# Kernel tuning notes

Hardware: AMD Instinct MI355X
Metric: run time of the kernel (lower is better)

## Reference

```python
import jax, jax.numpy as jnp
import numpy as np


def setup_inputs() -> dict:
    key = jax.random.key(0)
    k1, k2, k3, k4, k5 = jax.random.split(key, 5)
    B, T, N, F_IN, F_OUT, N_TYPES = 32, 128, 32, 256, 256, 8
    inp = jax.random.normal(k1, (B, T, N, F_IN), dtype=jnp.float32)
    g = jax.random.uniform(k2, (N, N), dtype=jnp.float32)
    node_type_index = jax.random.randint(k3, (N,), 0, N_TYPES, dtype=jnp.int64 if jax.config.read('jax_enable_x64') else jnp.int32)
    weight = jax.random.normal(k4, (N_TYPES, F_OUT, F_IN), dtype=jnp.float32) * (1.0 / np.sqrt(F_IN))
    bias = jax.random.normal(k5, (N_TYPES, F_OUT), dtype=jnp.float32) * 0.01
    return {"input": inp, "g": g, "node_type_index": node_type_index,
            "weight": weight, "bias": bias}


def reference(input, g, node_type_index, weight, bias):
    # Gather per-node weights/biases by node type.
    w = weight[node_type_index]            # [N, out, in]
    b = bias[node_type_index]              # [N, out]
    # Per-node linear: out[..., n, o] = sum_i input[..., n, i] * w[n, o, i]
    out = jnp.einsum('btni,noi->btno', input, w) + b  # [B, T, N, out]
    # Graph aggregation over node dim: g [N, N] @ out [..., N, out]
    out = jnp.einsum('mn,btno->btmo', g, out)
    return out
```

## Files before the change

kernel.cpp:

```cpp
#include <hip/hip_runtime.h>
#include <hip/hip_bf16.h>
#include <stdint.h>

typedef __bf16 bf16x8 __attribute__((ext_vector_type(8)));
typedef __bf16 bf16x4 __attribute__((ext_vector_type(4)));
typedef float f32x4 __attribute__((ext_vector_type(4)));

#define N_NODES 32
#define FDIM 256
#define N_TYPES 8
#define BT_TILE 32
#define TILES 16
#define ROW_B (FDIM * 2)

__device__ __forceinline__ unsigned swz(unsigned byte_off, unsigned row) {
    return byte_off ^ ((row & 7u) << 4);
}
__device__ __forceinline__ void lds_dma16(void* lds, const void* g) {
    __builtin_amdgcn_global_load_lds(
        (const __attribute__((address_space(1))) unsigned int*)g,
        (__attribute__((address_space(3))) unsigned int*)lds, 16, 0, 0);
}

__global__ __launch_bounds__(256) void k0_convert_w(
    const float* __restrict__ w, __bf16* __restrict__ wp)
{
    int idx = blockIdx.x * 256 + threadIdx.x;
    int t = idx >> 16, o = (idx >> 8) & 255, k = idx & 255;
    unsigned L = (unsigned)(o * ROW_B + k * 2) ^ ((o & 7u) << 4);
    wp[(size_t)t * (FDIM * FDIM) + (L >> 1)] = (__bf16)w[idx];
}

__global__ __launch_bounds__(256, 1) void k1_node_gemm(
    const float* __restrict__ input, const __bf16* __restrict__ wp,
    const float* __restrict__ bias, const int* __restrict__ ntype,
    char* __restrict__ outb)
{
    __shared__ __bf16 sW[FDIM * FDIM];
    __shared__ __bf16 sA[2][BT_TILE * FDIM];

    const int tid = threadIdx.x;
    const int n = blockIdx.x >> 3;
    const int base = (blockIdx.x & 7) * (TILES * BT_TILE);
    const int t = ntype[n];

    const int wid = tid >> 6, lane = tid & 63;
    const int lr = lane & 15, lq = lane >> 4;
    const int sr = tid >> 3;
    const int sk = tid & 7;

    char* sWb = (char*)sW;
    char* sA0 = (char*)sA[0];
    char* sA1 = (char*)sA[1];

    const char* wsrc = (const char*)(wp + (size_t)t * (FDIM * FDIM));
#pragma unroll
    for (int j = 0; j < 32; ++j)
        lds_dma16(sWb + j * 4096 + tid * 16, wsrc + j * 4096 + tid * 16);

    float bv[4];
#pragma unroll
    for (int nf = 0; nf < 4; ++nf)
        bv[nf] = bias[t * FDIM + wid * 64 + nf * 16 + lr];

    const char* Abase = (const char*)input
        + ((size_t)(base + sr) * (N_NODES * FDIM) + n * FDIM) * 4 + sk * 16;
    const size_t tile_stride = (size_t)BT_TILE * N_NODES * FDIM * 4;

    float4 av0[8], av1[8];
#pragma unroll
    for (int q = 0; q < 8; ++q)
        av0[q] = *reinterpret_cast<const float4*>(Abase + q * 128);
#pragma unroll
    for (int q = 0; q < 8; ++q)
        av1[q] = *reinterpret_cast<const float4*>(Abase + tile_stride + q * 128);

#pragma unroll
    for (int q = 0; q < 8; ++q) {
        bf16x4 h; h[0]=(__bf16)av0[q].x; h[1]=(__bf16)av0[q].y;
        h[2]=(__bf16)av0[q].z; h[3]=(__bf16)av0[q].w;
        *reinterpret_cast<bf16x4*>(sA0 + swz(sr * ROW_B + q * 64 + sk * 8, sr)) = h;
    }
    __syncthreads();

    f32x4 acc[2][4];

#define COMPUTE_TILE(SBUF, TI)                                                  \
    {                                                                           \
        _Pragma("unroll")                                                       \
        for (int mf = 0; mf < 2; ++mf)                                          \
            _Pragma("unroll")                                                   \
            for (int nf = 0; nf < 4; ++nf)                                      \
                acc[mf][nf] = f32x4{0.f, 0.f, 0.f, 0.f};                        \
        _Pragma("unroll")                                                       \
        for (int ks = 0; ks < 8; ++ks) {                                        \
            const int kb = ks * 64 + lq * 16;                                   \
            bf16x8 af[2], bfv[4];                                               \
            _Pragma("unroll")                                                   \
            for (int mf = 0; mf < 2; ++mf) {                                    \
                int r = mf * 16 + lr;                                           \
                af[mf] = *reinterpret_cast<const bf16x8*>(                      \
                    SBUF + swz(r * ROW_B + kb, r));                             \
            }                                                                   \
            _Pragma("unroll")                                                   \
            for (int nf = 0; nf < 4; ++nf) {                                    \
                int o = wid * 64 + nf * 16 + lr;                                \
                bfv[nf] = *reinterpret_cast<const bf16x8*>(                     \
                    sWb + swz(o * ROW_B + kb, o));                              \
            }                                                                   \
            _Pragma("unroll")                                                   \
            for (int mf = 0; mf < 2; ++mf)                                      \
                _Pragma("unroll")                                               \
                for (int nf = 0; nf < 4; ++nf)                                  \
                    acc[mf][nf] = __builtin_amdgcn_mfma_f32_16x16x32_bf16(      \
                        af[mf], bfv[nf], acc[mf][nf], 0, 0, 0);                 \
        }                                                                       \
                  \
        _Pragma("unroll")                                                       \
        for (int mf = 0; mf < 2; ++mf)                                          \
            _Pragma("unroll")                                                   \
            for (int j = 0; j < 4; ++j) {                                       \
                bf16x4 h;                                                       \
                _Pragma("unroll")                                               \
                for (int nf = 0; nf < 4; ++nf)                                  \
                    h[nf] = (__bf16)(acc[mf][nf][j] + bv[nf]);                  \
                size_t bt = (size_t)(base + (TI) * BT_TILE + mf * 16 + lq * 4 + j); \
                *reinterpret_cast<bf16x4*>(outb + bt * 32768 + n * 512          \
                                           + wid * 128 + lr * 8) = h;           \
            }                                                                   \
    }

#define CVT_TO(AV, SDST)                                                        \
    {                                                                           \
        _Pragma("unroll")                                                       \
        for (int q = 0; q < 8; ++q) {                                           \
            bf16x4 h; h[0]=(__bf16)AV[q].x; h[1]=(__bf16)AV[q].y;               \
            h[2]=(__bf16)AV[q].z; h[3]=(__bf16)AV[q].w;                         \
            *reinterpret_cast<bf16x4*>(SDST + swz(sr * ROW_B + q * 64 + sk * 8, \
                                                  sr)) = h;                     \
        }                                                                       \
    }

#define LOAD_TILE(AV, TI)                                                       \
    {                                                                           \
        const char* rp = Abase + (size_t)(TI) * tile_stride;                    \
        _Pragma("unroll")                                                       \
        for (int q = 0; q < 8; ++q)                                             \
            AV[q] = *reinterpret_cast<const float4*>(rp + q * 128);             \
    }

    for (int tt = 0; tt < 8; ++tt) {
        const int e = 2 * tt;
        if (e + 2 < TILES) LOAD_TILE(av0, e + 2);
        COMPUTE_TILE(sA0, e);
        CVT_TO(av1, sA1);
        __syncthreads();
        const int od = 2 * tt + 1;
        if (od + 2 < TILES) LOAD_TILE(av1, od + 2);
        COMPUTE_TILE(sA1, od);
        if (tt < 7) {
            CVT_TO(av0, sA0);
            __syncthreads();
        }
    }
#undef COMPUTE_TILE
#undef CVT_TO
#undef LOAD_TILE
}

__global__ __launch_bounds__(256) void k2_graph_agg(
    char* __restrict__ outb, const float* __restrict__ g)
{
    __shared__ float gs[N_NODES * N_NODES];
    const int tid = threadIdx.x;
    reinterpret_cast<float4*>(gs)[tid] = reinterpret_cast<const float4*>(g)[tid];

    const size_t bt = (size_t)blockIdx.x * 2 + (tid >> 7);
    const int c = tid & 127;
    const char* src = outb + bt * 32768 + c * 4;

    float vx[N_NODES], vy[N_NODES];
#pragma unroll
    for (int nn = 0; nn < N_NODES; ++nn) {
        unsigned d = *reinterpret_cast<const unsigned*>(src + nn * 512);
        union { unsigned u; float f; } c0, c1;
        c0.u = d << 16;
        c1.u = d & 0xffff0000u;
        vx[nn] = c0.f;
        vy[nn] = c1.f;
    }
    __syncthreads();

    const int o0 = (c >> 5) * 64 + (c & 1) * 32 + ((c >> 1) & 15);
    float* dst = (float*)(outb + bt * 32768) + o0;
#pragma unroll 4
    for (int m = 0; m < N_NODES; ++m) {
        float sx = 0.f, sy = 0.f;
#pragma unroll
        for (int nn = 0; nn < N_NODES; ++nn) {
            float gv = gs[m * N_NODES + nn];
            sx = fmaf(gv, vx[nn], sx);
            sy = fmaf(gv, vy[nn], sy);
        }
        dst[m * FDIM]      = sx;
        dst[m * FDIM + 16] = sy;
    }
}

extern "C" void kernel_launch(void* const* d_in, const int* in_sizes, int n_in,
                              void* d_out, int out_size, void* d_ws, size_t ws_size,
                              hipStream_t stream) {
    const float* input  = (const float*)d_in[0];
    const float* g      = (const float*)d_in[1];
    const int*   ntype  = (const int*)d_in[2];
    const float* weight = (const float*)d_in[3];
    const float* bias   = (const float*)d_in[4];
    char* outb = (char*)d_out;
    __bf16* wp = (__bf16*)d_ws;

    const int BT = in_sizes[0] / (N_NODES * FDIM);

    k0_convert_w<<<N_TYPES * FDIM * FDIM / 256, 256, 0, stream>>>(weight, wp);

    k1_node_gemm<<<N_NODES * 8, 256, 0, stream>>>(input, wp, bias, ntype, outb);

    k2_graph_agg<<<BT / 2, 256, 0, stream>>>(outb, g);
}
```

Measured before the change: 89.08 us.

## Stage packed bf16 intermediate in workspace, fall back to fp32 in-place path

When the workspace is large enough, the node GEMM writes its bf16 intermediate densely (16 KB per bt row) into a separate workspace region, and a new aggregation kernel reads it from there and writes the final output. Previously the intermediate sat half-packed inside the 32 KB output slots, so loads and stores shared the same lines. Otherwise the GEMM writes fp32 intermediates in place and a new per-slot aggregation kernel consumes them. The packed path halves the intermediate's footprint and keeps it from aliasing the output, at the cost of depending on workspace size.

```diff
diff --git a/kernel.cpp b/kernel.cpp
--- a/kernel.cpp
+++ b/kernel.cpp
@@ -12,6 +12,7 @@
 #define BT_TILE 32
 #define TILES 16
 #define ROW_B (FDIM * 2)
+#define WS_OFF (2u << 20)
 
 __device__ __forceinline__ unsigned swz(unsigned byte_off, unsigned row) {
     return byte_off ^ ((row & 7u) << 4);
@@ -31,10 +32,11 @@
     wp[(size_t)t * (FDIM * FDIM) + (L >> 1)] = (__bf16)w[idx];
 }
 
+template <bool PACKED>
 __global__ __launch_bounds__(256, 1) void k1_node_gemm(
     const float* __restrict__ input, const __bf16* __restrict__ wp,
     const float* __restrict__ bias, const int* __restrict__ ntype,
-    char* __restrict__ outb)
+    char* __restrict__ dst)
 {
     __shared__ __bf16 sW[FDIM * FDIM];
     __shared__ __bf16 sA[2][BT_TILE * FDIM];
@@ -115,18 +117,27 @@
                     acc[mf][nf] = __builtin_amdgcn_mfma_f32_16x16x32_bf16(      \
                         af[mf], bfv[nf], acc[mf][nf], 0, 0, 0);                 \
         }                                                                       \
-                  \
+                            \
         _Pragma("unroll")                                                       \
         for (int mf = 0; mf < 2; ++mf)                                          \
             _Pragma("unroll")                                                   \
             for (int j = 0; j < 4; ++j) {                                       \
-                bf16x4 h;                                                       \
-                _Pragma("unroll")                                               \
-                for (int nf = 0; nf < 4; ++nf)                                  \
-                    h[nf] = (__bf16)(acc[mf][nf][j] + bv[nf]);                  \
                 size_t bt = (size_t)(base + (TI) * BT_TILE + mf * 16 + lq * 4 + j); \
-                *reinterpret_cast<bf16x4*>(outb + bt * 32768 + n * 512          \
-                                           + wid * 128 + lr * 8) = h;           \
+                if constexpr (PACKED) {                                         \
+                    bf16x4 h;                                                   \
+                    _Pragma("unroll")                                           \
+                    for (int nf = 0; nf < 4; ++nf)                              \
+                        h[nf] = (__bf16)(acc[mf][nf][j] + bv[nf]);              \
+                    *reinterpret_cast<bf16x4*>(dst + bt * 16384 + n * 512       \
+                                               + wid * 128 + lr * 8) = h;       \
+                } else {                                                        \
+                    f32x4 h;                                                    \
+                    _Pragma("unroll")                                           \
+                    for (int nf = 0; nf < 4; ++nf)                              \
+                        h[nf] = acc[mf][nf][j] + bv[nf];                        \
+                    *reinterpret_cast<f32x4*>(dst + bt * 32768 + n * 1024       \
+                                              + wid * 256 + lr * 16) = h;       \
+                }                                                               \
             }                                                                   \
     }
 
@@ -168,8 +179,9 @@
 #undef LOAD_TILE
 }
 
-__global__ __launch_bounds__(256) void k2_graph_agg(
-    char* __restrict__ outb, const float* __restrict__ g)
+__global__ __launch_bounds__(256) void k2_packed(
+    const char* __restrict__ ws, char* __restrict__ outb,
+    const float* __restrict__ g)
 {
     __shared__ float gs[N_NODES * N_NODES];
     const int tid = threadIdx.x;
@@ -177,7 +189,7 @@
 
     const size_t bt = (size_t)blockIdx.x * 2 + (tid >> 7);
     const int c = tid & 127;
-    const char* src = outb + bt * 32768 + c * 4;
+    const char* src = ws + bt * 16384 + c * 4;
 
     float vx[N_NODES], vy[N_NODES];
 #pragma unroll
@@ -204,6 +216,36 @@
         }
         dst[m * FDIM]      = sx;
         dst[m * FDIM + 16] = sy;
+    }
+}
+
+__global__ __launch_bounds__(256) void k2_inplace(
+    char* __restrict__ outb, const float* __restrict__ g)
+{
+    __shared__ float gs[N_NODES * N_NODES];
+    const int tid = threadIdx.x;
+    reinterpret_cast<float4*>(gs)[tid] = reinterpret_cast<const float4*>(g)[tid];
+
+    char* slot = outb + (size_t)blockIdx.x * 32768;
+    const int o = tid;
+    const unsigned pbyte = ((unsigned)(o >> 6) << 8) + ((o & 15u) << 4)
+                         + (((o >> 4) & 3u) << 2);
+    const char* src = slot + pbyte;
+
+    float v[N_NODES];
+#pragma unroll
+    for (int nn = 0; nn < N_NODES; ++nn)
+        v[nn] = *reinterpret_cast<const float*>(src + nn * 1024);
+    __syncthreads();
+
+    float* dst = (float*)slot + o;
+#pragma unroll 4
+    for (int m = 0; m < N_NODES; ++m) {
+        float s = 0.f;
+#pragma unroll
+        for (int nn = 0; nn < N_NODES; ++nn)
+            s = fmaf(gs[m * N_NODES + nn], v[nn], s);
+        dst[m * FDIM] = s;
     }
 }
 
@@ -222,7 +264,15 @@
 
     k0_convert_w<<<N_TYPES * FDIM * FDIM / 256, 256, 0, stream>>>(weight, wp);
 
-    k1_node_gemm<<<N_NODES * 8, 256, 0, stream>>>(input, wp, bias, ntype, outb);
-
-    k2_graph_agg<<<BT / 2, 256, 0, stream>>>(outb, g);
-}
+    const size_t need = (size_t)WS_OFF + (size_t)BT * 16384;
+    if (ws_size >= need) {
+        char* wsmid = (char*)d_ws + WS_OFF;
+        k1_node_gemm<true><<<N_NODES * 8, 256, 0, stream>>>(
+            input, wp, bias, ntype, wsmid);
+        k2_packed<<<BT / 2, 256, 0, stream>>>(wsmid, outb, g);
+    } else {
+        k1_node_gemm<false><<<N_NODES * 8, 256, 0, stream>>>(
+            input, wp, bias, ntype, outb);
+        k2_inplace<<<BT, 256, 0, stream>>>(outb, g);
+    }
+}
```

Result: slower. 96.74 us (+8.6%).
